# Kernel tuning notes

Hardware: AMD Instinct MI355X
Metric: run time of the kernel (lower is better)

The kernel has to match this reference:

```python
import jax, jax.numpy as jnp
import numpy as np

N = 10000        # nodes
E = 640000       # edges (before self-loops)
IN = 128         # in_channels
HID = 32         # hidden_channels
HEADS = 4
HC = HID * HEADS # 128
OUT = 40         # out_channels
NEG_SLOPE = 0.2  # PyG GATConv default


def setup_inputs() -> dict:
    key = jax.random.key(0)
    ks = jax.random.split(key, 12)
    g = lambda k, shape: (jax.random.normal(k, shape, jnp.float32) * 0.1)
    return {
        "x": jax.random.normal(ks[0], (N, IN), jnp.float32),
        "edge_index": jax.random.randint(ks[1], (2, E), 0, N, dtype=jnp.int32),
        # conv1: in -> HID per head, HEADS heads, concat
        "W1": g(ks[2], (IN, HEADS * HID)),
        "a_src1": g(ks[3], (HEADS, HID)),
        "a_dst1": g(ks[4], (HEADS, HID)),
        "b1": jnp.zeros((HEADS * HID,), jnp.float32),
        # conv2: HC -> HC, 1 head
        "W2": g(ks[5], (HC, HC)),
        "a_src2": g(ks[6], (1, HC)),
        "a_dst2": g(ks[7], (1, HC)),
        "b2": jnp.zeros((HC,), jnp.float32),
        # final linear head
        "Wlin": g(ks[8], (HC, OUT)),
        "blin": jnp.zeros((OUT,), jnp.float32),
    }


def _gat_layer(x, W, a_src, a_dst, b, src, dst, heads, n):
    """PyG-style GATConv: gather -> edge attention -> segment softmax -> scatter."""
    d = W.shape[1] // heads
    h = (x @ W).reshape(n, heads, d)                       # [N, H, d]
    asrc = jnp.einsum('nhd,hd->nh', h, a_src)              # [N, H]
    adst = jnp.einsum('nhd,hd->nh', h, a_dst)
    e = jax.nn.leaky_relu(asrc[src] + adst[dst], NEG_SLOPE)  # [E, H]
    m = jax.ops.segment_max(e, dst, num_segments=n)          # per-dst max (stable softmax)
    p = jnp.exp(e - m[dst])
    z = jax.ops.segment_sum(p, dst, num_segments=n)
    alpha = p / (z[dst] + 1e-16)                             # [E, H]
    out = jax.ops.segment_sum(h[src] * alpha[:, :, None], dst, num_segments=n)
    return out.reshape(n, heads * d) + b


def reference(x, edge_index, W1, a_src1, a_dst1, b1, W2, a_src2, a_dst2, b2, Wlin, blin):
    n = x.shape[0]
    loop = jnp.arange(n, dtype=edge_index.dtype)           # add_self_loops=True
    src = jnp.concatenate([edge_index[0], loop])
    dst = jnp.concatenate([edge_index[1], loop])
    # eval mode: dropout is identity
    h1 = jax.nn.elu(_gat_layer(x, W1, a_src1, a_dst1, b1, src, dst, HEADS, n))
    h2 = jax.nn.elu(_gat_layer(h1, W2, a_src2, a_dst2, b2, src, dst, 1, n))
    return h2 @ Wlin + blin
```

## Files before the change

### kernel.cpp

```cpp
#include <hip/hip_runtime.h>
#include <hip/hip_bf16.h>

#define CAP 192

__global__ void fused_csr_gemm4(const int* __restrict__ srcArr, const int* __restrict__ dstArr,
                                int E, int N, int* __restrict__ deg, int* __restrict__ csr,
                                const float* __restrict__ x, const float* __restrict__ W,
                                const float* __restrict__ a_src, const float* __restrict__ a_dst,
                                __hip_bfloat16* __restrict__ hwb, float* __restrict__ asrc,
                                float* __restrict__ adst, int NG) {
    __shared__ float xr[8][128];
    int tid = threadIdx.x;
    if ((int)blockIdx.x >= NG) {
        int b = blockIdx.x - NG;
        int Etot = E + N;
        int base = b * 1024 + tid;
#pragma unroll
        for (int k = 0; k < 8; k++) {
            int i = base + k * 128;
            if (i < Etot) {
                int s, d;
                if (i < E) { s = srcArr[i]; d = dstArr[i]; }
                else       { s = d = i - E; }
                int p = atomicAdd(&deg[d], 1);
                if (p < CAP) csr[d * CAP + p] = s;
            }
        }
        return;
    }
    const int NB = 8;
    int n0 = blockIdx.x * NB;
    int j = tid;
    for (int r = 0; r < NB; r++) {
        int nn = n0 + r;
        xr[r][j] = (nn < N) ? x[nn * 128 + j] : 0.f;
    }
    __syncthreads();
    float acc[NB];
#pragma unroll
    for (int r = 0; r < NB; r++) acc[r] = 0.f;
    for (int k = 0; k < 128; k++) {
        float w = W[k * 128 + j];
#pragma unroll
        for (int r = 0; r < NB; r++) acc[r] += xr[r][k] * w;
    }
    int h = j >> 5;
    float as = a_src[j];
    float ad = a_dst[j];
    for (int r = 0; r < NB; r++) {
        int nn = n0 + r;
        if (nn < N) hwb[nn * 128 + j] = __float2bfloat16(acc[r]);
        float vs = acc[r] * as;
        float vd = acc[r] * ad;
        for (int off = 16; off >= 1; off >>= 1) {
            vs += __shfl_xor(vs, off);
            vd += __shfl_xor(vd, off);
        }
        if ((j & 31) == 0 && nn < N) { asrc[nn * 4 + h] = vs; adst[nn * 4 + h] = vd; }
    }
}

__global__ void gemm_att1(const float* __restrict__ x, const float* __restrict__ W,
                          const float* __restrict__ a_src, const float* __restrict__ a_dst,
                          __hip_bfloat16* __restrict__ hwb, float* __restrict__ asrc,
                          float* __restrict__ adst, int N) {
    const int NB = 8;
    int n0 = blockIdx.x * NB;
    int j = threadIdx.x;
    __shared__ float xr[NB][128];
    __shared__ float tmp[4];
    for (int r = 0; r < NB; r++) {
        int nn = n0 + r;
        xr[r][j] = (nn < N) ? x[nn * 128 + j] : 0.f;
    }
    __syncthreads();
    float acc[NB];
#pragma unroll
    for (int r = 0; r < NB; r++) acc[r] = 0.f;
    for (int k = 0; k < 128; k++) {
        float w = W[k * 128 + j];
#pragma unroll
        for (int r = 0; r < NB; r++) acc[r] += xr[r][k] * w;
    }
    float as = a_src[j];
    float ad = a_dst[j];
    for (int r = 0; r < NB; r++) {
        int nn = n0 + r;
        if (nn < N) hwb[nn * 128 + j] = __float2bfloat16(acc[r]);
        float vs = acc[r] * as;
        float vd = acc[r] * ad;
        for (int off = 32; off >= 1; off >>= 1) {
            vs += __shfl_xor(vs, off);
            vd += __shfl_xor(vd, off);
        }
        if ((j & 63) == 0) { tmp[(j >> 6) * 2] = vs; tmp[(j >> 6) * 2 + 1] = vd; }
        __syncthreads();
        if (j == 0 && nn < N) { asrc[nn] = tmp[0] + tmp[2]; adst[nn] = tmp[1] + tmp[3]; }
        __syncthreads();
    }
}

template <int H>
__global__ void agg(const __hip_bfloat16* __restrict__ hw, const float* __restrict__ asrc,
                    const float* __restrict__ adst, const int* __restrict__ degArr,
                    const int* __restrict__ csr_src, const float* __restrict__ b,
                    float* __restrict__ y, int N) {
    int n = blockIdx.x;
    int t = threadIdx.x;
    int g = t >> 5;
    int lane = t & 31;
    int beg = n * CAP;
    int deg = min(degArr[n], CAP);
    const unsigned short* hwu = (const unsigned short*)hw;
    __shared__ float pe[128 * H];
    __shared__ int se[128];
    __shared__ float adl[H];
    __shared__ float red[4 * 128];
    __shared__ float zred[2 * H];
    if (t < H) adl[t] = adst[n * H + t];
    const int dh = 128 / H;
    int hcol = (lane * 4) / dh;
    float4 acc = make_float4(0.f, 0.f, 0.f, 0.f);
    float zp[H];
#pragma unroll
    for (int hh = 0; hh < H; hh++) zp[hh] = 0.f;
    for (int base = 0; base < deg; base += 128) {
        int cnt = min(128, deg - base);
        __syncthreads();
        if (t < cnt) {
            int s = csr_src[beg + base + t];
            se[t] = s;
            if (H == 4) {
                float4 av = *(const float4*)&asrc[s * 4];
                float e0 = av.x + adl[0], e1 = av.y + adl[1];
                float e2 = av.z + adl[2], e3 = av.w + adl[3];
                e0 = e0 > 0.f ? e0 : 0.2f * e0;
                e1 = e1 > 0.f ? e1 : 0.2f * e1;
                e2 = e2 > 0.f ? e2 : 0.2f * e2;
                e3 = e3 > 0.f ? e3 : 0.2f * e3;
                float p0 = __expf(e0), p1 = __expf(e1), p2 = __expf(e2), p3 = __expf(e3);
                pe[t * 4 + 0] = p0; pe[t * 4 + 1] = p1;
                pe[t * 4 + 2] = p2; pe[t * 4 + 3] = p3;
                zp[0] += p0; zp[1] += p1; zp[2] += p2; zp[3] += p3;
            } else {
                float e = asrc[s] + adl[0];
                e = e > 0.f ? e : 0.2f * e;
                float p = __expf(e);
                pe[t] = p;
                zp[0] += p;
            }
        }
        __syncthreads();
        for (int c = g; c < cnt; c += 4) {
            int s = se[c];
            float p = pe[c * H + hcol];
            uint2 v = *(const uint2*)&hwu[s * 128 + lane * 4];
            float f0 = __uint_as_float(v.x << 16);
            float f1 = __uint_as_float(v.x & 0xffff0000u);
            float f2 = __uint_as_float(v.y << 16);
            float f3 = __uint_as_float(v.y & 0xffff0000u);
            acc.x += p * f0; acc.y += p * f1; acc.z += p * f2; acc.w += p * f3;
        }
    }
    ((float4*)&red[g * 128])[lane] = acc;
#pragma unroll
    for (int hh = 0; hh < H; hh++) {
        float v = zp[hh];
        for (int off = 32; off >= 1; off >>= 1) v += __shfl_xor(v, off);
        if ((t & 63) == 0) zred[(t >> 6) * H + hh] = v;
    }
    __syncthreads();
    float total = red[t] + red[128 + t] + red[256 + t] + red[384 + t];
    int h = t / dh;
    float z = zred[h] + zred[H + h];
    float res = total / (z + 1e-16f) + b[t];
    y[n * 128 + t] = res > 0.f ? res : (__expf(res) - 1.0f);
}

__global__ void lin_kernel(const float* __restrict__ y2, const float* __restrict__ Wl,
                           const float* __restrict__ bl, float* __restrict__ out,
                           int N, int OUTC) {
    const int NB = 8;
    int n0 = blockIdx.x * NB;
    int j = threadIdx.x;
    __shared__ float r[NB][128];
    for (int rr = 0; rr < NB; rr++) {
        int nn = n0 + rr;
        r[rr][j]      = (nn < N) ? y2[nn * 128 + j] : 0.f;
        r[rr][j + 64] = (nn < N) ? y2[nn * 128 + j + 64] : 0.f;
    }
    __syncthreads();
    if (j < OUTC) {
        float acc[NB];
#pragma unroll
        for (int rr = 0; rr < NB; rr++) acc[rr] = bl[j];
        for (int k = 0; k < 128; k++) {
            float w = Wl[k * OUTC + j];
#pragma unroll
            for (int rr = 0; rr < NB; rr++) acc[rr] += r[rr][k] * w;
        }
        for (int rr = 0; rr < NB; rr++) {
            int nn = n0 + rr;
            if (nn < N) out[nn * OUTC + j] = acc[rr];
        }
    }
}

extern "C" void kernel_launch(void* const* d_in, const int* in_sizes, int n_in,
                              void* d_out, int out_size, void* d_ws, size_t ws_size,
                              hipStream_t stream) {
    const float* x       = (const float*)d_in[0];
    const int*   ei      = (const int*)d_in[1];
    const float* W1      = (const float*)d_in[2];
    const float* a_src1  = (const float*)d_in[3];
    const float* a_dst1  = (const float*)d_in[4];
    const float* b1      = (const float*)d_in[5];
    const float* W2      = (const float*)d_in[6];
    const float* a_src2  = (const float*)d_in[7];
    const float* a_dst2  = (const float*)d_in[8];
    const float* b2      = (const float*)d_in[9];
    const float* Wlin    = (const float*)d_in[10];
    const float* blin    = (const float*)d_in[11];
    float* out = (float*)d_out;

    const int N = in_sizes[0] / 128;
    const int E = in_sizes[1] / 2;
    const int OUTC = in_sizes[10] / 128;
    const int Etot = E + N;
    const int* src = ei;
    const int* dst = ei + E;
    const int NG = (N + 7) / 8;
    const int NC = (Etot + 1023) / 1024;

    char* w = (char*)d_ws;
    size_t off = 0;
    auto alloc = [&](size_t bytes) -> char* {
        char* p = w + off;
        off += (bytes + 255) & ~(size_t)255;
        return p;
    };
    int*             deg   = (int*)alloc((size_t)N * 4);
    int*             csr   = (int*)alloc((size_t)N * CAP * 4);
    __hip_bfloat16*  hwb   = (__hip_bfloat16*)alloc((size_t)N * 128 * 2);
    float*           bufY  = (float*)alloc((size_t)N * 128 * 4);
    float*           asrc1 = (float*)alloc((size_t)N * 4 * 4);
    float*           adst1 = (float*)alloc((size_t)N * 4 * 4);
    float*           asrc2 = (float*)alloc((size_t)N * 4);
    float*           adst2 = (float*)alloc((size_t)N * 4);
    (void)ws_size;

    hipMemsetAsync(deg, 0, (size_t)N * 4, stream);
    fused_csr_gemm4<<<NG + NC, 128, 0, stream>>>(src, dst, E, N, deg, csr,
                                                 x, W1, a_src1, a_dst1, hwb, asrc1, adst1, NG);

    agg<4><<<N, 128, 0, stream>>>(hwb, asrc1, adst1, deg, csr, b1, bufY, N);

    gemm_att1<<<NG, 128, 0, stream>>>(bufY, W2, a_src2, a_dst2, hwb, asrc2, adst2, N);
    agg<1><<<N, 128, 0, stream>>>(hwb, asrc2, adst2, deg, csr, b2, bufY, N);

    lin_kernel<<<(N + 7) / 8, 64, 0, stream>>>(bufY, Wlin, blin, out, N, OUTC);
}
```

Measured before the change: 205.9 us.

## Fuse final linear into layer-2 aggregation and reorder CSR/GEMM blocks

```diff
diff --git a/kernel.cpp b/kernel.cpp
--- a/kernel.cpp
+++ b/kernel.cpp
@@ -8,15 +8,14 @@
                                 const float* __restrict__ x, const float* __restrict__ W,
                                 const float* __restrict__ a_src, const float* __restrict__ a_dst,
                                 __hip_bfloat16* __restrict__ hwb, float* __restrict__ asrc,
-                                float* __restrict__ adst, int NG) {
+                                float* __restrict__ adst, int NC) {
     __shared__ float xr[8][128];
     int tid = threadIdx.x;
-    if ((int)blockIdx.x >= NG) {
-        int b = blockIdx.x - NG;
+    if ((int)blockIdx.x < NC) {
         int Etot = E + N;
-        int base = b * 1024 + tid;
-#pragma unroll
-        for (int k = 0; k < 8; k++) {
+        int base = blockIdx.x * 512 + tid;
+#pragma unroll
+        for (int k = 0; k < 4; k++) {
             int i = base + k * 128;
             if (i < Etot) {
                 int s, d;
@@ -29,7 +28,7 @@
         return;
     }
     const int NB = 8;
-    int n0 = blockIdx.x * NB;
+    int n0 = (blockIdx.x - NC) * NB;
     int j = tid;
     for (int r = 0; r < NB; r++) {
         int nn = n0 + r;
@@ -100,11 +99,11 @@
     }
 }
 
-template <int H>
-__global__ void agg(const __hip_bfloat16* __restrict__ hw, const float* __restrict__ asrc,
-                    const float* __restrict__ adst, const int* __restrict__ degArr,
-                    const int* __restrict__ csr_src, const float* __restrict__ b,
-                    float* __restrict__ y, int N) {
+__global__ void agg4(const __hip_bfloat16* __restrict__ hw, const float* __restrict__ asrc,
+                     const float* __restrict__ adst, const int* __restrict__ degArr,
+                     const int* __restrict__ csr_src, const float* __restrict__ b,
+                     float* __restrict__ y, int N) {
+    const int H = 4;
     int n = blockIdx.x;
     int t = threadIdx.x;
     int g = t >> 5;
@@ -118,8 +117,7 @@
     __shared__ float red[4 * 128];
     __shared__ float zred[2 * H];
     if (t < H) adl[t] = adst[n * H + t];
-    const int dh = 128 / H;
-    int hcol = (lane * 4) / dh;
+    int hcol = lane >> 3;
     float4 acc = make_float4(0.f, 0.f, 0.f, 0.f);
     float zp[H];
 #pragma unroll
@@ -130,30 +128,22 @@
         if (t < cnt) {
             int s = csr_src[beg + base + t];
             se[t] = s;
-            if (H == 4) {
-                float4 av = *(const float4*)&asrc[s * 4];
-                float e0 = av.x + adl[0], e1 = av.y + adl[1];
-                float e2 = av.z + adl[2], e3 = av.w + adl[3];
-                e0 = e0 > 0.f ? e0 : 0.2f * e0;
-                e1 = e1 > 0.f ? e1 : 0.2f * e1;
-                e2 = e2 > 0.f ? e2 : 0.2f * e2;
-                e3 = e3 > 0.f ? e3 : 0.2f * e3;
-                float p0 = __expf(e0), p1 = __expf(e1), p2 = __expf(e2), p3 = __expf(e3);
-                pe[t * 4 + 0] = p0; pe[t * 4 + 1] = p1;
-                pe[t * 4 + 2] = p2; pe[t * 4 + 3] = p3;
-                zp[0] += p0; zp[1] += p1; zp[2] += p2; zp[3] += p3;
-            } else {
-                float e = asrc[s] + adl[0];
-                e = e > 0.f ? e : 0.2f * e;
-                float p = __expf(e);
-                pe[t] = p;
-                zp[0] += p;
-            }
+            float4 av = *(const float4*)&asrc[s * 4];
+            float e0 = av.x + adl[0], e1 = av.y + adl[1];
+            float e2 = av.z + adl[2], e3 = av.w + adl[3];
+            e0 = e0 > 0.f ? e0 : 0.2f * e0;
+            e1 = e1 > 0.f ? e1 : 0.2f * e1;
+            e2 = e2 > 0.f ? e2 : 0.2f * e2;
+            e3 = e3 > 0.f ? e3 : 0.2f * e3;
+            float p0 = __expf(e0), p1 = __expf(e1), p2 = __expf(e2), p3 = __expf(e3);
+            pe[t * 4 + 0] = p0; pe[t * 4 + 1] = p1;
+            pe[t * 4 + 2] = p2; pe[t * 4 + 3] = p3;
+            zp[0] += p0; zp[1] += p1; zp[2] += p2; zp[3] += p3;
         }
         __syncthreads();
         for (int c = g; c < cnt; c += 4) {
             int s = se[c];
-            float p = pe[c * H + hcol];
+            float p = pe[c * 4 + hcol];
             uint2 v = *(const uint2*)&hwu[s * 128 + lane * 4];
             float f0 = __uint_as_float(v.x << 16);
             float f1 = __uint_as_float(v.x & 0xffff0000u);
@@ -171,38 +161,73 @@
     }
     __syncthreads();
     float total = red[t] + red[128 + t] + red[256 + t] + red[384 + t];
-    int h = t / dh;
+    int h = t >> 5;
     float z = zred[h] + zred[H + h];
     float res = total / (z + 1e-16f) + b[t];
     y[n * 128 + t] = res > 0.f ? res : (__expf(res) - 1.0f);
 }
 
-__global__ void lin_kernel(const float* __restrict__ y2, const float* __restrict__ Wl,
-                           const float* __restrict__ bl, float* __restrict__ out,
-                           int N, int OUTC) {
-    const int NB = 8;
-    int n0 = blockIdx.x * NB;
-    int j = threadIdx.x;
-    __shared__ float r[NB][128];
-    for (int rr = 0; rr < NB; rr++) {
-        int nn = n0 + rr;
-        r[rr][j]      = (nn < N) ? y2[nn * 128 + j] : 0.f;
-        r[rr][j + 64] = (nn < N) ? y2[nn * 128 + j + 64] : 0.f;
-    }
-    __syncthreads();
-    if (j < OUTC) {
-        float acc[NB];
-#pragma unroll
-        for (int rr = 0; rr < NB; rr++) acc[rr] = bl[j];
-        for (int k = 0; k < 128; k++) {
-            float w = Wl[k * OUTC + j];
-#pragma unroll
-            for (int rr = 0; rr < NB; rr++) acc[rr] += r[rr][k] * w;
-        }
-        for (int rr = 0; rr < NB; rr++) {
-            int nn = n0 + rr;
-            if (nn < N) out[nn * OUTC + j] = acc[rr];
-        }
+__global__ void agg1_lin(const __hip_bfloat16* __restrict__ hw, const float* __restrict__ asrc,
+                         const float* __restrict__ adst, const int* __restrict__ degArr,
+                         const int* __restrict__ csr_src, const float* __restrict__ b,
+                         const float* __restrict__ Wl, const float* __restrict__ bl,
+                         float* __restrict__ out, int N, int OUTC) {
+    int n = blockIdx.x;
+    int t = threadIdx.x;
+    int g = t >> 5;
+    int lane = t & 31;
+    int beg = n * CAP;
+    int deg = min(degArr[n], CAP);
+    const unsigned short* hwu = (const unsigned short*)hw;
+    __shared__ float pe[128];
+    __shared__ int se[128];
+    __shared__ float adl;
+    __shared__ float red[4 * 128];
+    __shared__ float zred[2];
+    __shared__ float yrow[128];
+    if (t == 0) adl = adst[n];
+    float4 acc = make_float4(0.f, 0.f, 0.f, 0.f);
+    float zp = 0.f;
+    for (int base = 0; base < deg; base += 128) {
+        int cnt = min(128, deg - base);
+        __syncthreads();
+        if (t < cnt) {
+            int s = csr_src[beg + base + t];
+            se[t] = s;
+            float e = asrc[s] + adl;
+            e = e > 0.f ? e : 0.2f * e;
+            float p = __expf(e);
+            pe[t] = p;
+            zp += p;
+        }
+        __syncthreads();
+        for (int c = g; c < cnt; c += 4) {
+            int s = se[c];
+            float p = pe[c];
+            uint2 v = *(const uint2*)&hwu[s * 128 + lane * 4];
+            float f0 = __uint_as_float(v.x << 16);
+            float f1 = __uint_as_float(v.x & 0xffff0000u);
+            float f2 = __uint_as_float(v.y << 16);
+            float f3 = __uint_as_float(v.y & 0xffff0000u);
+            acc.x += p * f0; acc.y += p * f1; acc.z += p * f2; acc.w += p * f3;
+        }
+    }
+    ((float4*)&red[g * 128])[lane] = acc;
+    {
+        float v = zp;
+        for (int off = 32; off >= 1; off >>= 1) v += __shfl_xor(v, off);
+        if ((t & 63) == 0) zred[t >> 6] = v;
+    }
+    __syncthreads();
+    float total = red[t] + red[128 + t] + red[256 + t] + red[384 + t];
+    float z = zred[0] + zred[1];
+    float res = total / (z + 1e-16f) + b[t];
+    yrow[t] = res > 0.f ? res : (__expf(res) - 1.0f);
+    __syncthreads();
+    if (t < OUTC) {
+        float a = bl[t];
+        for (int k = 0; k < 128; k++) a += yrow[k] * Wl[k * OUTC + t];
+        out[n * OUTC + t] = a;
     }
 }
 
@@ -230,7 +255,7 @@
     const int* src = ei;
     const int* dst = ei + E;
     const int NG = (N + 7) / 8;
-    const int NC = (Etot + 1023) / 1024;
+    const int NC = (Etot + 511) / 512;
 
     char* w = (char*)d_ws;
     size_t off = 0;
@@ -250,13 +275,11 @@
     (void)ws_size;
 
     hipMemsetAsync(deg, 0, (size_t)N * 4, stream);
-    fused_csr_gemm4<<<NG + NC, 128, 0, stream>>>(src, dst, E, N, deg, csr,
-                                                 x, W1, a_src1, a_dst1, hwb, asrc1, adst1, NG);
-
-    agg<4><<<N, 128, 0, stream>>>(hwb, asrc1, adst1, deg, csr, b1, bufY, N);
+    fused_csr_gemm4<<<NC + NG, 128, 0, stream>>>(src, dst, E, N, deg, csr,
+                                                 x, W1, a_src1, a_dst1, hwb, asrc1, adst1, NC);
+
+    agg4<<<N, 128, 0, stream>>>(hwb, asrc1, adst1, deg, csr, b1, bufY, N);
 
     gemm_att1<<<NG, 128, 0, stream>>>(bufY, W2, a_src2, a_dst2, hwb, asrc2, adst2, N);
-    agg<1><<<N, 128, 0, stream>>>(hwb, asrc2, adst2, deg, csr, b2, bufY, N);
-
-    lin_kernel<<<(N + 7) / 8, 64, 0, stream>>>(bufY, Wlin, blin, out, N, OUTC);
-}
+    agg1_lin<<<N, 128, 0, stream>>>(hwb, asrc2, adst2, deg, csr, b2, Wlin, blin, out, N, OUTC);
+}
```

Result: no change. 204.4 us (-0.8%).
